# Kernel optimization log

Measured on AMD Instinct MI355X. Metric: run time of the kernel, lower is better.

The kernel has to match this reference:

```python
import jax, jax.numpy as jnp
import numpy as np
import math

B, S, D, H = 4, 2048, 1024, 16
HD = D // H  # head_size = 64


def setup_inputs() -> dict:
    key = jax.random.key(0)
    ks = jax.random.split(key, 12)
    s = 1.0 / math.sqrt(D)
    inp = {
        "query_in": jax.random.normal(ks[0], (B, S, D), jnp.float32),
        "key_in": jax.random.normal(ks[1], (B, S, D), jnp.float32),
        "values_in": jax.random.normal(ks[2], (B, S, D), jnp.float32),
        # causal mask, broadcast over batch and heads
        "mask": jnp.tril(jnp.ones((S, S), jnp.int32))[None, None],
        "Wq": jax.random.normal(ks[3], (D, D), jnp.float32) * s,
        "bq": jnp.zeros((D,), jnp.float32),
        "Wk": jax.random.normal(ks[4], (D, D), jnp.float32) * s,
        "bk": jnp.zeros((D,), jnp.float32),
        "Wv": jax.random.normal(ks[5], (D, D), jnp.float32) * s,
        "bv": jnp.zeros((D,), jnp.float32),
        "Wo": jax.random.normal(ks[6], (D, D), jnp.float32) * s,
        "bo": jnp.zeros((D,), jnp.float32),
    }
    return inp


def _heads(x):
    # [B,S,D] -> [B,H,S,HD]
    return x.reshape(B, S, H, HD).transpose(0, 2, 1, 3)


def reference(query_in, key_in, values_in, mask, Wq, bq, Wk, bk, Wv, bv, Wo, bo):
    q = _heads(query_in @ Wq.T + bq)
    k = _heads(key_in @ Wk.T + bk)
    v = _heads(values_in @ Wv.T + bv)
    # scaled dot-product scores [B,H,Sq,Sk]
    att = jnp.einsum("bhqd,bhkd->bhqk", q, k) / math.sqrt(HD)
    att = jnp.where(mask == 0, jnp.float32(-1e9), att)
    # NOTE: original module applies dropout (identity at eval / p=0) directly
    # to scores with NO softmax -- faithfully reproduced here.
    out = jnp.einsum("bhqk,bhkd->bhqd", att, v)
    out = out.transpose(0, 2, 1, 3).reshape(B, S, D)
    return out @ Wo.T + bo
```

## Files before the change

### kernel.cpp

```cpp
#include <hip/hip_runtime.h>
#include <stdint.h>

typedef unsigned short ushort_t;
typedef __bf16 bf16x8 __attribute__((ext_vector_type(8)));
typedef float f32x4 __attribute__((ext_vector_type(4)));
typedef ushort_t us4 __attribute__((ext_vector_type(4)));

#define MFMA16(a, b, c) __builtin_amdgcn_mfma_f32_16x16x32_bf16((a), (b), (c), 0, 0, 0)

constexpr int Bn = 4, Sn = 2048, Dn = 1024, Hn = 16, HDn = 64;
constexpr float SCALE = 0.125f;
constexpr float NEG = -1e9f;

__device__ __forceinline__ float bf2f(ushort_t u) {
  unsigned x = ((unsigned)u) << 16;
  return __builtin_bit_cast(float, x);
}
__device__ __forceinline__ ushort_t f2bf(float f) {
  unsigned x = __builtin_bit_cast(unsigned, f);
  x = x + 0x7FFFu + ((x >> 16) & 1u);
  return (ushort_t)(x >> 16);
}
__device__ __forceinline__ uint4 ld8_f32_bf16(const float* __restrict__ p) {
  float4 a = *(const float4*)p;
  float4 b = *(const float4*)(p + 4);
  union { ushort_t u[8]; uint4 v; } r;
  r.u[0] = f2bf(a.x); r.u[1] = f2bf(a.y); r.u[2] = f2bf(a.z); r.u[3] = f2bf(a.w);
  r.u[4] = f2bf(b.x); r.u[5] = f2bf(b.y); r.u[6] = f2bf(b.z); r.u[7] = f2bf(b.w);
  return r.v;
}
__device__ __forceinline__ void gl2lds16(const void* g, void* l) {
  __builtin_amdgcn_global_load_lds(
      (__attribute__((address_space(1))) void*)g,
      (__attribute__((address_space(3))) void*)l, 16, 0, 0);
}

__global__ __launch_bounds__(256)
void cvt_all(const float* __restrict__ xq, const float* __restrict__ xk,
             const float* __restrict__ xv, const float* __restrict__ wq,
             const float* __restrict__ wk, const float* __restrict__ wv,
             const float* __restrict__ wo, ushort_t* __restrict__ Xd,
             ushort_t* __restrict__ Wd) {
  const unsigned stride = gridDim.x * 256;
  for (unsigned c = blockIdx.x * 256 + threadIdx.x; c < 3670016u; c += stride) {
    if (c < 3145728u) {
      const unsigned which = c >> 20;
      const float* s = which == 0 ? xq : which == 1 ? xk : xv;
      size_t i = (size_t)(c & 1048575u) * 8;
      *(uint4*)(Xd + (size_t)which * 8388608 + i) = ld8_f32_bf16(s + i);
    } else {
      const unsigned wc = c - 3145728u;
      const unsigned which = wc >> 17;
      const float* s = which == 0 ? wq : which == 1 ? wk : which == 2 ? wv : wo;
      size_t i = (size_t)(wc & 131071u) * 8;
      *(uint4*)(Wd + (size_t)which * 1048576 + i) = ld8_f32_bf16(s + i);
    }
  }
}

__global__ __launch_bounds__(256, 4)
void gemm_proj(const ushort_t* __restrict__ A, const ushort_t* __restrict__ Wt,
               const float* __restrict__ bias, ushort_t* __restrict__ Cp,
               float* __restrict__ Rs, const int mode) {
  constexpr int K = 1024;
  __shared__ __align__(16) ushort_t As[128 * 64];
  __shared__ __align__(16) ushort_t Bs[128 * 64];

  const int tid = threadIdx.x;
  const int lane = tid & 63, w = tid >> 6;
  const int quad = lane >> 4, l16 = lane & 15;
  const int wm = w >> 1, wn = w & 1;
  const int row0 = blockIdx.x * 128;
  const int col0 = blockIdx.y * 128;

  const int sr = lane >> 3;
  const int sg = ((lane & 7) ^ (sr & 7)) * 8;
  const ushort_t* Ab = A  + (size_t)(row0 + w * 32 + sr) * K + sg;
  const ushort_t* Bb = Wt + (size_t)(col0 + w * 32 + sr) * K + sg;

  f32x4 acc[4][4] = {};

  for (int k0 = 0; k0 < K; k0 += 64) {
    __syncthreads();
#pragma unroll
    for (int i = 0; i < 4; ++i) {
      gl2lds16(Ab + (size_t)(i * 8) * K + k0, &As[(w * 32 + i * 8) * 64]);
      gl2lds16(Bb + (size_t)(i * 8) * K + k0, &Bs[(w * 32 + i * 8) * 64]);
    }
    __syncthreads();
#pragma unroll
    for (int ks = 0; ks < 2; ++ks) {
      const int kg = ((ks * 4 + quad) ^ (l16 & 7)) * 8;
      bf16x8 af[4], bfr[4];
#pragma unroll
      for (int mt = 0; mt < 4; ++mt)
        af[mt] = *(const bf16x8*)(&As[(wm * 64 + mt * 16 + l16) * 64 + kg]);
#pragma unroll
      for (int nt = 0; nt < 4; ++nt)
        bfr[nt] = *(const bf16x8*)(&Bs[(wn * 64 + nt * 16 + l16) * 64 + kg]);
#pragma unroll
      for (int mt = 0; mt < 4; ++mt)
#pragma unroll
        for (int nt = 0; nt < 4; ++nt)
          acc[mt][nt] = MFMA16(af[mt], bfr[nt], acc[mt][nt]);
    }
  }

#pragma unroll
  for (int mt = 0; mt < 4; ++mt) {
#pragma unroll
    for (int nt = 0; nt < 4; ++nt) {
      const int col = col0 + wn * 64 + nt * 16 + l16;
      const float bv4 = bias[col];
      const int rowb = row0 + wm * 64 + mt * 16 + quad * 4;
      if (mode != 0) {
        const int b = rowb >> 11, s = rowb & (Sn - 1);
        const int h = col >> 6, hd = col & 63;
        us4 pk;
#pragma unroll
        for (int r = 0; r < 4; ++r) pk[r] = f2bf(acc[mt][nt][r] + bv4);
        *(us4*)(Cp + ((size_t)((b * Hn + h) * HDn + hd)) * Sn + s) = pk;
      } else {
#pragma unroll
        for (int r = 0; r < 4; ++r) {
          const int row = rowb + r;
          const int b = row >> 11, s = row & (Sn - 1);
          const int h = col >> 6, hd = col & 63;
          Cp[(((size_t)(b * Hn + h) * Sn + s) << 6) + hd] = f2bf(acc[mt][nt][r] + bv4);
        }
      }
    }
  }

  if (mode == 2) {
    const int b = row0 >> 11;
    const int t = ((row0 & (Sn - 1)) >> 6) + wm;
#pragma unroll
    for (int nt = 0; nt < 4; ++nt) {
      const int col = col0 + wn * 64 + nt * 16 + l16;
      const float bv4 = bias[col];
      float p = 0.f;
#pragma unroll
      for (int mt = 0; mt < 4; ++mt)
#pragma unroll
        for (int r = 0; r < 4; ++r) p += acc[mt][nt][r] + bv4;
      p += __shfl_xor(p, 16);
      p += __shfl_xor(p, 32);
      if (quad == 0) {
        const int h = col >> 6, n = col & 63;
        Rs[((size_t)(b * Hn + h) * 32 + t) * 64 + n] = p;
      }
    }
  }
}

__global__ __launch_bounds__(256, 4)
void gemm_out(const ushort_t* __restrict__ A, const ushort_t* __restrict__ Wt,
              const float* __restrict__ bias, float* __restrict__ Cp) {
  constexpr int K = 1024;
  __shared__ __align__(16) ushort_t As[128 * 64];
  __shared__ __align__(16) ushort_t Bs[128 * 64];

  const int tid = threadIdx.x;
  const int lane = tid & 63, w = tid >> 6;
  const int quad = lane >> 4, l16 = lane & 15;
  const int wm = w >> 1, wn = w & 1;
  const int row0 = blockIdx.x * 128;
  const int col0 = blockIdx.y * 128;

  const int sr = lane >> 3;
  const int sg = ((lane & 7) ^ (sr & 7)) * 8;
  const ushort_t* Ab = A  + (size_t)(row0 + w * 32 + sr) * K + sg;
  const ushort_t* Bb = Wt + (size_t)(col0 + w * 32 + sr) * K + sg;

  f32x4 acc[4][4] = {};

  for (int k0 = 0; k0 < K; k0 += 64) {
    __syncthreads();
#pragma unroll
    for (int i = 0; i < 4; ++i) {
      gl2lds16(Ab + (size_t)(i * 8) * K + k0, &As[(w * 32 + i * 8) * 64]);
      gl2lds16(Bb + (size_t)(i * 8) * K + k0, &Bs[(w * 32 + i * 8) * 64]);
    }
    __syncthreads();
#pragma unroll
    for (int ks = 0; ks < 2; ++ks) {
      const int kg = ((ks * 4 + quad) ^ (l16 & 7)) * 8;
      bf16x8 af[4], bfr[4];
#pragma unroll
      for (int mt = 0; mt < 4; ++mt)
        af[mt] = *(const bf16x8*)(&As[(wm * 64 + mt * 16 + l16) * 64 + kg]);
#pragma unroll
      for (int nt = 0; nt < 4; ++nt)
        bfr[nt] = *(const bf16x8*)(&Bs[(wn * 64 + nt * 16 + l16) * 64 + kg]);
#pragma unroll
      for (int mt = 0; mt < 4; ++mt)
#pragma unroll
        for (int nt = 0; nt < 4; ++nt)
          acc[mt][nt] = MFMA16(af[mt], bfr[nt], acc[mt][nt]);
    }
  }

#pragma unroll
  for (int mt = 0; mt < 4; ++mt)
#pragma unroll
    for (int nt = 0; nt < 4; ++nt) {
      const int col = col0 + wn * 64 + nt * 16 + l16;
      const float bv = bias[col];
      const int rowb = row0 + wm * 64 + mt * 16 + quad * 4;
#pragma unroll
      for (int r = 0; r < 4; ++r)
        Cp[(size_t)(rowb + r) * 1024 + col] = acc[mt][nt][r] + bv;
    }
}

__global__ __launch_bounds__(256)
void scan_attn2(const ushort_t* __restrict__ Q, const ushort_t* __restrict__ Kt,
                const ushort_t* __restrict__ Vt, const float* __restrict__ Rs,
                ushort_t* __restrict__ O) {
  __shared__ __align__(16) char smem[51200];
  ushort_t* KpB  = (ushort_t*)smem;
  ushort_t* Zs   = (ushort_t*)(smem + 8192);
  ushort_t* VtsB = (ushort_t*)(smem + 16384);
  ushort_t* Ks   = (ushort_t*)(smem + 32768);
  ushort_t (*Ss)[72] = (ushort_t(*)[72])(smem + 40960);
  float (*sfx)[64] = (float(*)[64])(smem + 50176);

  const int tid = threadIdx.x, lane = tid & 63, w = tid >> 6;
  const int quad = lane >> 4, l16 = lane & 15;
  const int bh = blockIdx.x;
  const int g = blockIdx.y;
  const int qt0 = g * 4;
  const int b = bh >> 4, h = bh & 15;
  const ushort_t* Qb  = Q  + (size_t)bh * Sn * HDn;
  const ushort_t* Ktb = Kt + (size_t)bh * HDn * Sn;
  const ushort_t* Vtb = Vt + (size_t)bh * HDn * Sn;
  const float* Rb = Rs + (size_t)bh * 32 * 64;

  const int sr = lane >> 3;
  const int sg = ((lane & 7) ^ (sr & 7)) * 8;
  const int q8 = lane & 7, h8 = lane >> 3;

  f32x4 pzacc[4] = {};
  if (qt0 > 0) {
#pragma unroll
    for (int c = 0; c < 2; ++c) {
      const int row = w * 16 + c * 8;
      gl2lds16(Ktb + (size_t)(row + sr) * Sn + sg, &KpB[row * 64]);
      gl2lds16(Vtb + (size_t)(row + sr) * Sn + sg, &VtsB[row * 64]);
    }
    for (int tau = 0; tau < qt0; ++tau) {
      const int pc = tau & 1;
      __syncthreads();
      if (tau + 1 < qt0) {
#pragma unroll
        for (int c = 0; c < 2; ++c) {
          const int row = w * 16 + c * 8;
          gl2lds16(Ktb + (size_t)(row + sr) * Sn + (tau + 1) * 64 + sg,
                   &KpB[(1 - pc) * 4096 + row * 64]);
          gl2lds16(Vtb + (size_t)(row + sr) * Sn + (tau + 1) * 64 + sg,
                   &VtsB[(1 - pc) * 4096 + row * 64]);
        }
      }
#pragma unroll
      for (int ks = 0; ks < 2; ++ks) {
        const int kg = ((ks * 4 + quad) ^ (l16 & 7)) * 8;
        bf16x8 ak = *(const bf16x8*)(&KpB[pc * 4096 + (w * 16 + l16) * 64 + kg]);
#pragma unroll
        for (int nt = 0; nt < 4; ++nt) {
          bf16x8 bv8 = *(const bf16x8*)(&VtsB[pc * 4096 + (nt * 16 + l16) * 64 + kg]);
          pzacc[nt] = MFMA16(ak, bv8, pzacc[nt]);
        }
      }
    }
    __syncthreads();
  }

  uint4  kvr[2][2];
  bf16x8 bqr[2][2];
  {
    const int q0 = qt0 * 64;
#pragma unroll
    for (int c = 0; c < 2; ++c) {
      const int row = w * 16 + c * 8;
      gl2lds16(Vtb + (size_t)(row + sr) * Sn + q0 + sg, &VtsB[row * 64]);
      kvr[0][c] = *(const uint4*)(Ktb + (size_t)(w * 16 + c * 8 + h8) * Sn + q0 + q8 * 8);
    }
#pragma unroll
    for (int ks = 0; ks < 2; ++ks)
      bqr[0][ks] = *(const bf16x8*)(Qb + (size_t)(q0 + w * 16 + l16) * HDn + (ks * 4 + quad) * 8);
  }

  if (tid < 64) {
    float acc = 0.f;
    for (int tau = 31; tau >= qt0; --tau) {
      if (tau < qt0 + 4) sfx[tau - qt0][tid] = acc;
      acc += Rb[(size_t)tau * 64 + tid];
    }
  }

#pragma unroll 4
  for (int i = 0; i < 4; ++i) {
    const int cur = i & 1;
    const int qt = qt0 + i, q0 = qt * 64;

    __syncthreads();

#pragma unroll
    for (int nt = 0; nt < 4; ++nt) {
      const int n = nt * 16 + l16;
      const int d0 = w * 16 + quad * 4;
      us4 pk;
#pragma unroll
      for (int r = 0; r < 4; ++r) pk[r] = f2bf(SCALE * pzacc[nt][r]);
      *(us4*)(&Zs[n * 64 + (((d0 >> 3) ^ (n & 7)) << 3) + (d0 & 7)]) = pk;
    }
#pragma unroll
    for (int c = 0; c < 2; ++c) {
      const int hd = w * 16 + c * 8 + h8;
      const int G = hd >> 3;
      const ushort_t* ku = (const ushort_t*)&kvr[cur][c];
#pragma unroll
      for (int j = 0; j < 8; ++j) {
        const int e = (j + q8) & 7;
        const int s = q8 * 8 + e;
        Ks[s * 64 + ((G ^ e) << 3) + (hd & 7)] = ku[e];
      }
    }
#pragma unroll
    for (int c = 0; c < 2; ++c) {
      const int hd = w * 16 + c * 8 + h8;
      *(uint4*)(&KpB[hd * 64 + ((q8 ^ (hd & 7)) << 3)]) = kvr[cur][c];
    }

    __syncthreads();

    if (i < 3) {
      const int q1 = (qt + 1) * 64, nxt = 1 - cur;
#pragma unroll
      for (int c = 0; c < 2; ++c) {
        const int row = w * 16 + c * 8;
        gl2lds16(Vtb + (size_t)(row + sr) * Sn + q1 + sg, &VtsB[nxt * 4096 + row * 64]);
        kvr[nxt][c] = *(const uint4*)(Ktb + (size_t)(w * 16 + c * 8 + h8) * Sn + q1 + q8 * 8);
      }
#pragma unroll
      for (int ks = 0; ks < 2; ++ks)
        bqr[nxt][ks] = *(const bf16x8*)(Qb + (size_t)(q1 + w * 16 + l16) * HDn + (ks * 4 + quad) * 8);
    }

    f32x4 oacc[4] = {};
#pragma unroll
    for (int ks = 0; ks < 2; ++ks) {
      const int kg = ((ks * 4 + quad) ^ (l16 & 7)) * 8;
#pragma unroll
      for (int nt = 0; nt < 4; ++nt) {
        bf16x8 az = *(const bf16x8*)(&Zs[(nt * 16 + l16) * 64 + kg]);
        oacc[nt] = MFMA16(az, bqr[cur][ks], oacc[nt]);
      }
    }
    f32x4 sacc[4] = {};
#pragma unroll
    for (int ks = 0; ks < 2; ++ks) {
      const int kg = ((ks * 4 + quad) ^ (l16 & 7)) * 8;
#pragma unroll
      for (int nt = 0; nt < 4; ++nt) {
        bf16x8 ak = *(const bf16x8*)(&Ks[(nt * 16 + l16) * 64 + kg]);
        sacc[nt] = MFMA16(ak, bqr[cur][ks], sacc[nt]);
      }
    }
    const int qrel = w * 16 + l16;
#pragma unroll
    for (int nt = 0; nt < 4; ++nt) {
      const int kb = nt * 16 + quad * 4;
      us4 pk;
#pragma unroll
      for (int r = 0; r < 4; ++r) {
        float val = (kb + r > qrel) ? NEG : sacc[nt][r] * SCALE;
        pk[r] = f2bf(val);
      }
      *(us4*)(&Ss[qrel][kb]) = pk;
    }
#pragma unroll
    for (int ks = 0; ks < 2; ++ks) {
      bf16x8 bs = *(const bf16x8*)(&Ss[qrel][ks * 32 + quad * 8]);
#pragma unroll
      for (int nt = 0; nt < 4; ++nt) {
        bf16x8 av = *(const bf16x8*)(&VtsB[cur * 4096 + (nt * 16 + l16) * 64 + (((ks * 4 + quad) ^ (l16 & 7)) << 3)]);
        oacc[nt] = MFMA16(av, bs, oacc[nt]);
      }
    }

    const int s = q0 + w * 16 + l16;
#pragma unroll
    for (int nt = 0; nt < 4; ++nt) {
      const int nb = nt * 16 + quad * 4;
      float4 s4 = *(const float4*)(&sfx[i][nb]);
      us4 pk;
      pk[0] = f2bf(oacc[nt][0] + NEG * s4.x);
      pk[1] = f2bf(oacc[nt][1] + NEG * s4.y);
      pk[2] = f2bf(oacc[nt][2] + NEG * s4.z);
      pk[3] = f2bf(oacc[nt][3] + NEG * s4.w);
      *(us4*)(&O[((size_t)(b * Sn + s)) * Dn + h * 64 + nb]) = pk;
    }

    if (i < 3) {
#pragma unroll
      for (int ks = 0; ks < 2; ++ks) {
        const int kg = ((ks * 4 + quad) ^ (l16 & 7)) * 8;
        bf16x8 ak = *(const bf16x8*)(&KpB[(w * 16 + l16) * 64 + kg]);
#pragma unroll
        for (int nt = 0; nt < 4; ++nt) {
          bf16x8 bv8 = *(const bf16x8*)(&VtsB[cur * 4096 + (nt * 16 + l16) * 64 + kg]);
          pzacc[nt] = MFMA16(ak, bv8, pzacc[nt]);
        }
      }
    }
  }
}

extern "C" void kernel_launch(void* const* d_in, const int* in_sizes, int n_in,
                              void* d_out, int out_size, void* d_ws, size_t ws_size,
                              hipStream_t stream) {
  const float* Xq = (const float*)d_in[0];
  const float* Xk = (const float*)d_in[1];
  const float* Xv = (const float*)d_in[2];
  const float* Wq = (const float*)d_in[4];
  const float* bq = (const float*)d_in[5];
  const float* Wk = (const float*)d_in[6];
  const float* bk = (const float*)d_in[7];
  const float* Wv = (const float*)d_in[8];
  const float* bv = (const float*)d_in[9];
  const float* Wo = (const float*)d_in[10];
  const float* bo = (const float*)d_in[11];

  constexpr size_t MiB = 1024 * 1024;
  char* ws = (char*)d_ws;
  ushort_t* Xb  = (ushort_t*)(ws);
  ushort_t* Wb  = (ushort_t*)(ws + 48 * MiB);
  ushort_t* Qb  = (ushort_t*)(ws + 56 * MiB);
  ushort_t* Ktb = (ushort_t*)(ws + 72 * MiB);
  ushort_t* Vtb = (ushort_t*)(ws + 88 * MiB);
  ushort_t* Ob  = (ushort_t*)(ws + 120 * MiB);
  float*    Rsum= (float*)   (ws + 176 * MiB);

  cvt_all<<<2048, 256, 0, stream>>>(Xq, Xk, Xv, Wq, Wk, Wv, Wo, Xb, Wb);
  gemm_proj<<<dim3(64, 8), 256, 0, stream>>>(Xb, Wb, bq, Qb, Rsum, 0);
  gemm_proj<<<dim3(64, 8), 256, 0, stream>>>(Xb + (size_t)1 * 8388608,
                                             Wb + (size_t)1 * 1048576, bk, Ktb,
                                             Rsum, 1);
  gemm_proj<<<dim3(64, 8), 256, 0, stream>>>(Xb + (size_t)2 * 8388608,
                                             Wb + (size_t)2 * 1048576, bv, Vtb,
                                             Rsum, 2);
  scan_attn2<<<dim3(64, 8), 256, 0, stream>>>(Qb, Ktb, Vtb, Rsum, Ob);
  gemm_out<<<dim3(64, 8), 256, 0, stream>>>(Ob, Wb + (size_t)3 * 1048576, bo,
                                            (float*)d_out);
}
```

Before: 306.9 us.

## Fuse fp32-to-bf16 conversion into QKV GEMM and merge three projection launches

Removes the separate conversion kernel. The projection GEMM now loads fp32 inputs and weights directly, converts them to bf16 in registers and writes them to LDS, prefetching the next K tile into registers. The three Q/K/V projections run as one launch over grid z, and the Wo conversion is folded into the attention kernel. This avoids a full bf16 round trip of the activations through memory and two launches, but replaces async global-to-LDS loads with register-staged fp32 loads that double the per-tile bytes and raise register pressure.

Result: slower. 672.1 us (+119.0%).

```diff
diff --git a/kernel.cpp b/kernel.cpp
--- a/kernel.cpp
+++ b/kernel.cpp
@@ -12,14 +12,16 @@
 constexpr float SCALE = 0.125f;
 constexpr float NEG = -1e9f;
 
-__device__ __forceinline__ float bf2f(ushort_t u) {
-  unsigned x = ((unsigned)u) << 16;
-  return __builtin_bit_cast(float, x);
-}
 __device__ __forceinline__ ushort_t f2bf(float f) {
   unsigned x = __builtin_bit_cast(unsigned, f);
   x = x + 0x7FFFu + ((x >> 16) & 1u);
   return (ushort_t)(x >> 16);
+}
+__device__ __forceinline__ bf16x8 cvt8(float4 a, float4 b) {
+  bf16x8 r;
+  r[0] = (__bf16)a.x; r[1] = (__bf16)a.y; r[2] = (__bf16)a.z; r[3] = (__bf16)a.w;
+  r[4] = (__bf16)b.x; r[5] = (__bf16)b.y; r[6] = (__bf16)b.z; r[7] = (__bf16)b.w;
+  return r;
 }
 __device__ __forceinline__ uint4 ld8_f32_bf16(const float* __restrict__ p) {
   float4 a = *(const float4*)p;
@@ -35,36 +37,23 @@
       (__attribute__((address_space(3))) void*)l, 16, 0, 0);
 }
 
-__global__ __launch_bounds__(256)
-void cvt_all(const float* __restrict__ xq, const float* __restrict__ xk,
+__global__ __launch_bounds__(256, 4)
+void qkv_f32(const float* __restrict__ xq, const float* __restrict__ xk,
              const float* __restrict__ xv, const float* __restrict__ wq,
              const float* __restrict__ wk, const float* __restrict__ wv,
-             const float* __restrict__ wo, ushort_t* __restrict__ Xd,
-             ushort_t* __restrict__ Wd) {
-  const unsigned stride = gridDim.x * 256;
-  for (unsigned c = blockIdx.x * 256 + threadIdx.x; c < 3670016u; c += stride) {
-    if (c < 3145728u) {
-      const unsigned which = c >> 20;
-      const float* s = which == 0 ? xq : which == 1 ? xk : xv;
-      size_t i = (size_t)(c & 1048575u) * 8;
-      *(uint4*)(Xd + (size_t)which * 8388608 + i) = ld8_f32_bf16(s + i);
-    } else {
-      const unsigned wc = c - 3145728u;
-      const unsigned which = wc >> 17;
-      const float* s = which == 0 ? wq : which == 1 ? wk : which == 2 ? wv : wo;
-      size_t i = (size_t)(wc & 131071u) * 8;
-      *(uint4*)(Wd + (size_t)which * 1048576 + i) = ld8_f32_bf16(s + i);
-    }
-  }
-}
-
-__global__ __launch_bounds__(256, 4)
-void gemm_proj(const ushort_t* __restrict__ A, const ushort_t* __restrict__ Wt,
-               const float* __restrict__ bias, ushort_t* __restrict__ Cp,
-               float* __restrict__ Rs, const int mode) {
+             const float* __restrict__ bq, const float* __restrict__ bk,
+             const float* __restrict__ bv, ushort_t* __restrict__ Qd,
+             ushort_t* __restrict__ Ktd, ushort_t* __restrict__ Vtd,
+             float* __restrict__ Rs) {
   constexpr int K = 1024;
   __shared__ __align__(16) ushort_t As[128 * 64];
   __shared__ __align__(16) ushort_t Bs[128 * 64];
+
+  const int z = blockIdx.z;
+  const float* A  = z == 0 ? xq : z == 1 ? xk : xv;
+  const float* Wf = z == 0 ? wq : z == 1 ? wk : wv;
+  const float* bias = z == 0 ? bq : z == 1 ? bk : bv;
+  ushort_t* Cp = z == 0 ? Qd : z == 1 ? Ktd : Vtd;
 
   const int tid = threadIdx.x;
   const int lane = tid & 63, w = tid >> 6;
@@ -73,10 +62,21 @@
   const int row0 = blockIdx.x * 128;
   const int col0 = blockIdx.y * 128;
 
-  const int sr = lane >> 3;
-  const int sg = ((lane & 7) ^ (sr & 7)) * 8;
-  const ushort_t* Ab = A  + (size_t)(row0 + w * 32 + sr) * K + sg;
-  const ushort_t* Bb = Wt + (size_t)(col0 + w * 32 + sr) * K + sg;
+  const int ar = lane >> 3;
+  const int ac = (lane & 7) * 8;
+  const float* Af = A  + (size_t)(row0 + w * 32 + ar) * K + ac;
+  const float* Bf = Wf + (size_t)(col0 + w * 32 + ar) * K + ac;
+  ushort_t* Adst = &As[(w * 32 + ar) * 64 + (((lane & 7) ^ (ar & 7)) * 8)];
+  ushort_t* Bdst = &Bs[(w * 32 + ar) * 64 + (((lane & 7) ^ (ar & 7)) * 8)];
+
+  float4 a0[4], a1[4], b0[4], b1[4];
+#pragma unroll
+  for (int i = 0; i < 4; ++i) {
+    const float* sa = Af + (size_t)(i * 8) * K;
+    const float* sb = Bf + (size_t)(i * 8) * K;
+    a0[i] = *(const float4*)sa; a1[i] = *(const float4*)(sa + 4);
+    b0[i] = *(const float4*)sb; b1[i] = *(const float4*)(sb + 4);
+  }
 
   f32x4 acc[4][4] = {};
 
@@ -84,10 +84,21 @@
     __syncthreads();
 #pragma unroll
     for (int i = 0; i < 4; ++i) {
-      gl2lds16(Ab + (size_t)(i * 8) * K + k0, &As[(w * 32 + i * 8) * 64]);
-      gl2lds16(Bb + (size_t)(i * 8) * K + k0, &Bs[(w * 32 + i * 8) * 64]);
-    }
-    __syncthreads();
+      *(bf16x8*)(Adst + i * 8 * 64) = cvt8(a0[i], a1[i]);
+      *(bf16x8*)(Bdst + i * 8 * 64) = cvt8(b0[i], b1[i]);
+    }
+    __syncthreads();
+
+    if (k0 + 64 < K) {
+#pragma unroll
+      for (int i = 0; i < 4; ++i) {
+        const float* sa = Af + (size_t)(i * 8) * K + (k0 + 64);
+        const float* sb = Bf + (size_t)(i * 8) * K + (k0 + 64);
+        a0[i] = *(const float4*)sa; a1[i] = *(const float4*)(sa + 4);
+        b0[i] = *(const float4*)sb; b1[i] = *(const float4*)(sb + 4);
+      }
+    }
+
 #pragma unroll
     for (int ks = 0; ks < 2; ++ks) {
       const int kg = ((ks * 4 + quad) ^ (l16 & 7)) * 8;
@@ -113,7 +124,7 @@
       const int col = col0 + wn * 64 + nt * 16 + l16;
       const float bv4 = bias[col];
       const int rowb = row0 + wm * 64 + mt * 16 + quad * 4;
-      if (mode != 0) {
+      if (z != 0) {
         const int b = rowb >> 11, s = rowb & (Sn - 1);
         const int h = col >> 6, hd = col & 63;
         us4 pk;
@@ -132,7 +143,7 @@
     }
   }
 
-  if (mode == 2) {
+  if (z == 2) {
     const int b = row0 >> 11;
     const int t = ((row0 & (Sn - 1)) >> 6) + wm;
 #pragma unroll
@@ -217,6 +228,7 @@
 __global__ __launch_bounds__(256)
 void scan_attn2(const ushort_t* __restrict__ Q, const ushort_t* __restrict__ Kt,
                 const ushort_t* __restrict__ Vt, const float* __restrict__ Rs,
+                const float* __restrict__ wo, ushort_t* __restrict__ WoB,
                 ushort_t* __restrict__ O) {
   __shared__ __align__(16) char smem[51200];
   ushort_t* KpB  = (ushort_t*)smem;
@@ -240,6 +252,11 @@
   const int sr = lane >> 3;
   const int sg = ((lane & 7) ^ (sr & 7)) * 8;
   const int q8 = lane & 7, h8 = lane >> 3;
+
+  {
+    const size_t i = ((size_t)(bh * 8 + g) * 256 + tid) * 8;
+    *(uint4*)(WoB + i) = ld8_f32_bf16(wo + i);
+  }
 
   f32x4 pzacc[4] = {};
   if (qt0 > 0) {
@@ -435,23 +452,15 @@
 
   constexpr size_t MiB = 1024 * 1024;
   char* ws = (char*)d_ws;
-  ushort_t* Xb  = (ushort_t*)(ws);
-  ushort_t* Wb  = (ushort_t*)(ws + 48 * MiB);
-  ushort_t* Qb  = (ushort_t*)(ws + 56 * MiB);
-  ushort_t* Ktb = (ushort_t*)(ws + 72 * MiB);
-  ushort_t* Vtb = (ushort_t*)(ws + 88 * MiB);
-  ushort_t* Ob  = (ushort_t*)(ws + 120 * MiB);
-  float*    Rsum= (float*)   (ws + 176 * MiB);
-
-  cvt_all<<<2048, 256, 0, stream>>>(Xq, Xk, Xv, Wq, Wk, Wv, Wo, Xb, Wb);
-  gemm_proj<<<dim3(64, 8), 256, 0, stream>>>(Xb, Wb, bq, Qb, Rsum, 0);
-  gemm_proj<<<dim3(64, 8), 256, 0, stream>>>(Xb + (size_t)1 * 8388608,
-                                             Wb + (size_t)1 * 1048576, bk, Ktb,
-                                             Rsum, 1);
-  gemm_proj<<<dim3(64, 8), 256, 0, stream>>>(Xb + (size_t)2 * 8388608,
-                                             Wb + (size_t)2 * 1048576, bv, Vtb,
-                                             Rsum, 2);
-  scan_attn2<<<dim3(64, 8), 256, 0, stream>>>(Qb, Ktb, Vtb, Rsum, Ob);
-  gemm_out<<<dim3(64, 8), 256, 0, stream>>>(Ob, Wb + (size_t)3 * 1048576, bo,
-                                            (float*)d_out);
-}
+  ushort_t* Qb  = (ushort_t*)(ws);
+  ushort_t* Ktb = (ushort_t*)(ws + 16 * MiB);
+  ushort_t* Vtb = (ushort_t*)(ws + 32 * MiB);
+  ushort_t* Ob  = (ushort_t*)(ws + 48 * MiB);
+  ushort_t* WoB = (ushort_t*)(ws + 64 * MiB);
+  float*    Rsum= (float*)   (ws + 66 * MiB);
+
+  qkv_f32<<<dim3(64, 8, 3), 256, 0, stream>>>(Xq, Xk, Xv, Wq, Wk, Wv,
+                                              bq, bk, bv, Qb, Ktb, Vtb, Rsum);
+  scan_attn2<<<dim3(64, 8), 256, 0, stream>>>(Qb, Ktb, Vtb, Rsum, Wo, WoB, Ob);
+  gemm_out<<<dim3(64, 8), 256, 0, stream>>>(Ob, WoB, bo, (float*)d_out);
+}
```
